# Performance work log

Hardware: AMD Instinct MI355X
Metric: run time of the kernel (lower is better)

The kernel has to match this reference:

```python
import jax, jax.numpy as jnp
import numpy as np

B, S, T = 256, 512, 20
VOCAB, E, H, SKIP = 100000, 25, 128, 64


def _lstm_scan(x, skip, mask, K, R, Sk, b):
    # x:[S,B,E], skip:[S,B,SKIP], mask:[S,B] bool. Keras RNN mask semantics:
    # masked steps carry previous h/c and emit previous h.
    Bn = x.shape[1]
    Hn = R.shape[0]
    def step(carry, inp):
        h, c = carry
        xt, st, mt = inp
        z = xt @ K + h @ R + st @ Sk + b            # [B,4H]
        zi, zf, zg, zo = jnp.split(z, 4, axis=-1)
        cn = jax.nn.sigmoid(zf) * c + jax.nn.sigmoid(zi) * jnp.tanh(zg)
        hn = jax.nn.sigmoid(zo) * jnp.tanh(cn)
        m = mt[:, None]
        h2 = jnp.where(m, hn, h)
        c2 = jnp.where(m, cn, c)
        return (h2, c2), h2
    init = (jnp.zeros((Bn, Hn), x.dtype), jnp.zeros((Bn, Hn), x.dtype))
    (hF, cF), hs = jax.lax.scan(step, init, (x, skip, mask))
    return hs, hF


def setup_inputs() -> dict:
    key = jax.random.key(0)
    ks = jax.random.split(key, 20)
    p = lambda k, shp: jax.random.normal(k, shp, dtype=jnp.float32) * 0.05
    inp = {
        "input_tags": jax.random.randint(ks[0], (B, S, T), 0, VOCAB, dtype=jnp.int32),
        "embedded_skips": jax.random.normal(ks[1], (B, S, SKIP), dtype=jnp.float32),
        "emb_table": p(ks[2], (VOCAB, E)),
        "kernel_f": p(ks[3], (E, 4 * H)),
        "rec_f": p(ks[4], (H, 4 * H)),
        "skip_f": p(ks[5], (SKIP, 4 * H)),
        "bias_f": jnp.zeros((4 * H,), jnp.float32),
        "kernel_b": p(ks[6], (E, 4 * H)),
        "rec_b": p(ks[7], (H, 4 * H)),
        "skip_b": p(ks[8], (SKIP, 4 * H)),
        "bias_b": jnp.zeros((4 * H,), jnp.float32),
        "Wk": p(ks[9], (2 * H, H)),
        "bk": jnp.zeros((H,), jnp.float32),
        "Wq": p(ks[10], (H, H)),
        "bq": jnp.zeros((H,), jnp.float32),
        "We": p(ks[11], (H, 1)),
        "be": jnp.zeros((1,), jnp.float32),
    }
    return inp


def reference(input_tags, embedded_skips, emb_table,
              kernel_f, rec_f, skip_f, bias_f,
              kernel_b, rec_b, skip_b, bias_b,
              Wk, bk, Wq, bq, We, be):
    mask3 = input_tags != 0                          # [B,S,T]
    emb = emb_table[input_tags]                      # [B,S,T,E]
    num_mask = mask3.astype(emb.dtype)
    summed = jnp.sum(emb * num_mask[..., None], axis=2)   # [B,S,E]
    denom = jnp.sum(num_mask, axis=2)                     # [B,S]
    denom = jnp.where(denom == 0, jnp.ones_like(denom), denom)
    gru_inp = summed / denom[..., None]                   # [B,S,E]
    step_mask = mask3[:, :, 0]                            # [B,S]

    # time-major for scan
    x_t = jnp.swapaxes(gru_inp, 0, 1)
    s_t = jnp.swapaxes(embedded_skips, 0, 1)
    m_t = jnp.swapaxes(step_mask, 0, 1)

    hs_f, h_fwd = _lstm_scan(x_t, s_t, m_t, kernel_f, rec_f, skip_f, bias_f)
    hs_b_rev, _ = _lstm_scan(x_t[::-1], s_t[::-1], m_t[::-1], kernel_b, rec_b, skip_b, bias_b)
    hs_b = hs_b_rev[::-1]
    out = jnp.swapaxes(jnp.concatenate([hs_f, hs_b], axis=-1), 0, 1)  # [B,S,2H]

    keys = out @ Wk + bk                                  # [B,S,H]
    queries = (h_fwd @ Wq + bq)[:, None, :]               # [B,1,H]
    energy = jnp.tanh(keys + queries) @ We + be           # [B,S,1]
    energy = energy + (1.0 - step_mask.astype(energy.dtype))[..., None] * -1e9
    weights = jax.nn.softmax(energy, axis=1)
    context = jnp.sum(weights * out, axis=1)              # [B,2H]
    return context
```

## Files before the change

### kernel.cpp

```cpp
#include <hip/hip_runtime.h>
#include <math.h>

#define Bb 256
#define Ss 512
#define Tt 20
#define Ee 25
#define Hh 128
#define SKIPn 64
#define H4n 512
#define BSn (Bb*Ss)
#define MG 4
#define HP 160
#define ZP 520
#define AP 264
#define LOG2E 1.4426950408889634f

typedef _Float16 f16x8 __attribute__((ext_vector_type(8)));
typedef _Float16 f16x4 __attribute__((ext_vector_type(4)));
typedef float f32x4 __attribute__((ext_vector_type(4)));

__device__ __forceinline__ float rcpf(float x) { return __builtin_amdgcn_rcpf(x); }
__device__ __forceinline__ float exp2f_(float x) { return __builtin_amdgcn_exp2f(x); }

__device__ __forceinline__ void lgkm_barrier() {
    __asm__ __volatile__("" ::: "memory");
    __builtin_amdgcn_s_waitcnt(0xC07F);
    __builtin_amdgcn_s_barrier();
    __asm__ __volatile__("" ::: "memory");
}

__global__ void pool_kernel(const int* __restrict__ tags,
                            const float* __restrict__ table,
                            _Float16* __restrict__ gru16, float* __restrict__ maskf,
                            float* __restrict__ maskt) {
    int group = blockIdx.x * 8 + (threadIdx.x >> 5);
    int lane = threadIdx.x & 31;
    if (group >= BSn) return;
    int b = group >> 9;
    int t = group & (Ss - 1);
    const int* tg = tags + (size_t)group * Tt;
    const int el = (lane < Ee) ? lane : (Ee - 1);

    int tagv[Tt];
#pragma unroll
    for (int tt = 0; tt < Tt; tt++) tagv[tt] = tg[tt];

    float vv[Tt];
#pragma unroll
    for (int tt = 0; tt < Tt; tt++)
        vv[tt] = table[(size_t)tagv[tt] * Ee + el];

    float acc = 0.0f;
    int cnt = 0;
#pragma unroll
    for (int tt = 0; tt < Tt; tt++) {
        const bool nz = (tagv[tt] != 0);
        cnt += nz ? 1 : 0;
        acc += nz ? vv[tt] : 0.0f;
    }
    float scale = rcpf((float)(cnt > 0 ? cnt : 1));
    float v = (lane < Ee) ? acc * scale : 0.0f;
    gru16[((size_t)t * Bb + b) * 32 + lane] = (_Float16)v;
    if (lane == 0) {
        float m = (tagv[0] != 0) ? 1.0f : 0.0f;
        maskf[group] = m;
        maskt[(size_t)t * Bb + b] = m;
    }
}

__global__ void __launch_bounds__(256)
cvt_kernel(const float* __restrict__ in, _Float16* __restrict__ out) {
    size_t i = ((size_t)blockIdx.x * 256 + threadIdx.x) * 8;
    f32x4 a = *(const f32x4*)(in + i);
    f32x4 b = *(const f32x4*)(in + i + 4);
    f16x8 o;
#pragma unroll
    for (int j = 0; j < 4; j++) { o[j] = (_Float16)a[j]; o[j + 4] = (_Float16)b[j]; }
    *(f16x8*)(out + i) = o;
}

__global__ void __launch_bounds__(512)
__attribute__((amdgpu_waves_per_eu(2, 2)))
scan_kernel(const _Float16* __restrict__ gru16, const _Float16* __restrict__ sk16,
            const float* __restrict__ maskt,
            const float* __restrict__ Kf, const float* __restrict__ Rf,
            const float* __restrict__ Skf, const float* __restrict__ bf,
            const float* __restrict__ Kb, const float* __restrict__ Rb,
            const float* __restrict__ Skb, const float* __restrict__ bb,
            _Float16* __restrict__ hs16, float* __restrict__ hfwd)
{
    __shared__ __align__(16) _Float16 h16[2 * MG * HP];
    __shared__ __align__(16) _Float16 zlds[64 * ZP];

    const int tid = threadIdx.x;
    const int lane = tid & 63;
    const int w = tid >> 6;
    const int l16 = lane & 15;
    const int q = lane >> 4;
    const int mb = l16 >> 2;
    const int bg = blockIdx.x & 63;
    const int dir = blockIdx.x >> 6;
    const int b0 = bg * MG;
    const int col = 16 * w + l16;

    const float* Kw = dir ? Kb : Kf;
    const float* Rw = dir ? Rb : Rf;
    const float* Sw = dir ? Skb : Skf;
    const float* bw = dir ? bb : bf;
    const float gs[4] = {LOG2E, LOG2E, 2.0f * LOG2E, LOG2E};

    f16x8 hfr[4][4];
#pragma unroll
    for (int kt = 0; kt < 4; kt++) {
#pragma unroll
        for (int g = 0; g < 4; g++) {
            const int n = g * Hh + col;
            f16x8 v;
#pragma unroll
            for (int j = 0; j < 8; j++)
                v[j] = (_Float16)(Rw[(32 * kt + 8 * q + j) * H4n + n] * gs[g]);
            hfr[kt][g] = v;
        }
    }
    f16x8 bx[4], bs0[4], bs1[4];
    f32x4 biasA[4];
#pragma unroll
    for (int g = 0; g < 4; g++) {
        const int n = g * Hh + col;
        f16x8 vx, v0, v1;
#pragma unroll
        for (int j = 0; j < 8; j++) {
            const int kk = 8 * q + j;
            vx[j] = (_Float16)(((kk < Ee) ? Kw[kk * H4n + n] : 0.0f) * gs[g]);
            v0[j] = (_Float16)(Sw[kk * H4n + n] * gs[g]);
            v1[j] = (_Float16)(Sw[(32 + kk) * H4n + n] * gs[g]);
        }
        bx[g] = vx; bs0[g] = v0; bs1[g] = v1;
        const float bv = bw[g * Hh + col] * gs[g];
        f32x4 ba = {bv, bv, bv, bv};
        biasA[g] = ba;
    }
    const f32x4 zacc4 = {0.0f, 0.0f, 0.0f, 0.0f};

    for (int idx = tid; idx < 2 * MG * HP; idx += 512) h16[idx] = (_Float16)0.0f;

    float c = 0.0f, h = 0.0f;

    const int tsub = l16 >> 2, bbn = l16 & 3;
    const int tg0 = dir ? (Ss - 1 - tsub) : tsub;
    const _Float16* px = gru16 + ((size_t)tg0 * Bb + b0 + bbn) * 32 + 8 * q;
    const _Float16* ps = sk16 + ((size_t)(b0 + bbn) * Ss + tg0) * SKIPn + 8 * q;
    const ptrdiff_t pxd = (dir ? -4 : 4) * (ptrdiff_t)(Bb * 32);
    const ptrdiff_t psd = (dir ? -4 : 4) * (ptrdiff_t)SKIPn;

    const float* mptr = maskt + (size_t)(dir ? (Ss - 1) : 0) * Bb + b0 + q;
    const ptrdiff_t mdelta = dir ? -(ptrdiff_t)Bb : (ptrdiff_t)Bb;
    float mA = mptr[0], mB = mptr[mdelta];
    const float* mpf = mptr + 2 * mdelta;

    _Float16* hsp = hs16 + ((size_t)(b0 + q) * Ss + (dir ? Ss - 1 : 0)) * (2 * Hh)
                    + dir * Hh + col;
    const ptrdiff_t odelta = dir ? -(2 * Hh) : (2 * Hh);

    f16x8 nax = *(const f16x8*)px;
    f16x8 na0 = *(const f16x8*)ps;
    f16x8 na1 = *(const f16x8*)(ps + 32);

    __syncthreads();

    auto body = [&](int i, float& mkv) {
        const _Float16* hb = h16 + (i & 1) * (MG * HP);
        const f16x8 ah0 = *(const f16x8*)(hb + mb * HP +  0 + 8 * q);
        const f16x8 ah1 = *(const f16x8*)(hb + mb * HP + 32 + 8 * q);
        const f16x8 ah2 = *(const f16x8*)(hb + mb * HP + 64 + 8 * q);
        const f16x8 ah3 = *(const f16x8*)(hb + mb * HP + 96 + 8 * q);
        const f16x4 z4 = *(const f16x4*)(zlds + ((i & 15) * 4 + q) * ZP + col * 4);

        f32x4 acc[4];
#pragma unroll
        for (int g = 0; g < 4; g++) {
            acc[g] = __builtin_amdgcn_mfma_f32_16x16x32_f16(ah0, hfr[0][g], zacc4, 0, 0, 0);
            acc[g] = __builtin_amdgcn_mfma_f32_16x16x32_f16(ah1, hfr[1][g], acc[g], 0, 0, 0);
            acc[g] = __builtin_amdgcn_mfma_f32_16x16x32_f16(ah2, hfr[2][g], acc[g], 0, 0, 0);
            acc[g] = __builtin_amdgcn_mfma_f32_16x16x32_f16(ah3, hfr[3][g], acc[g], 0, 0, 0);
        }

        const float mk = mkv;
        mkv = *mpf; mpf += mdelta;
        const float zi = acc[0][0] + (float)z4[0];
        const float zf = acc[1][0] + (float)z4[1];
        const float zg = acc[2][0] + (float)z4[2];
        const float zo = acc[3][0] + (float)z4[3];
        const float ei = exp2f_(fminf(-zi, 88.0f));
        const float ef = exp2f_(fminf(-zf, 88.0f));
        const float eg = exp2f_(fminf(-zg, 88.0f));
        const float eo = exp2f_(fminf(-zo, 88.0f));
        const float pi = 1.0f + ei, pg = 1.0f + eg, pf = 1.0f + ef;
        const float p  = pi * pg;
        const float t1 = (1.0f - eg) * pf;
        const float cn = fmaf(c, p, t1) * rcpf(pf * p);
        const float ec = exp2f_(fminf(cn * (-2.0f * LOG2E), 88.0f));
        const float hn = (1.0f - ec) * rcpf((1.0f + eo) * (1.0f + ec));
        const bool mm = (mk != 0.0f);
        c = mm ? cn : c;
        h = mm ? hn : h;

        _Float16* hw = h16 + ((i + 1) & 1) * (MG * HP);
        hw[q * HP + col] = (_Float16)h;
        *hsp = (_Float16)h;
        hsp += odelta;
        lgkm_barrier();
    };

    int i = 0;
#pragma unroll 1
    for (int k = 0; k < 32; ++k) {
#pragma unroll
        for (int tile = 0; tile < 4; ++tile) {
            const f16x8 ax = nax, a0 = na0, a1 = na1;
            px += pxd; ps += psd;
            if ((k < 31) | (tile < 3)) {
                nax = *(const f16x8*)px;
                na0 = *(const f16x8*)ps;
                na1 = *(const f16x8*)(ps + 32);
            }
            f32x4 zc[4];
#pragma unroll
            for (int g = 0; g < 4; g++) {
                zc[g] = __builtin_amdgcn_mfma_f32_16x16x32_f16(ax, bx[g],  biasA[g], 0, 0, 0);
                zc[g] = __builtin_amdgcn_mfma_f32_16x16x32_f16(a0, bs0[g], zc[g], 0, 0, 0);
                zc[g] = __builtin_amdgcn_mfma_f32_16x16x32_f16(a1, bs1[g], zc[g], 0, 0, 0);
            }
            _Float16* zw = zlds + ((tile * 4 + q) * 4) * ZP + col * 4;
#pragma unroll
            for (int r = 0; r < 4; r++) {
                f16x4 o;
                o[0] = (_Float16)zc[0][r]; o[1] = (_Float16)zc[1][r];
                o[2] = (_Float16)zc[2][r]; o[3] = (_Float16)zc[3][r];
                *(f16x4*)(zw + r * ZP) = o;
            }
        }
        lgkm_barrier();
#pragma unroll 1
        for (int j = 0; j < 16; j += 2) {
            body(i,     mA);
            body(i + 1, mB);
            i += 2;
        }
    }

    if (dir == 0) hfwd[(size_t)(b0 + q) * Hh + col] = h;
}

__global__ void __launch_bounds__(512)
attn_kernel(const _Float16* __restrict__ hs16, const float* __restrict__ hfwd,
            const float* __restrict__ Wq, const float* __restrict__ bq,
            const float* __restrict__ bk,
            const float* __restrict__ Wk, const float* __restrict__ We,
            const float* __restrict__ maskf, float* __restrict__ outp)
{
    __shared__ float hfl[Hh];
    __shared__ float qpart[4][Hh];
    __shared__ float qtot_s[Hh];
    __shared__ float epart[8][Ss];
    __shared__ float ws2[Ss];
    __shared__ float redm[8], reds[8];
    __shared__ float ctxp[16][2 * Hh + 1];
    __shared__ __align__(16) _Float16 atile[2][16 * AP];

    const int tid = threadIdx.x;
    const int lane = tid & 63;
    const int w = tid >> 6;
    const int l16 = lane & 15;
    const int q = lane >> 4;
    const int b = blockIdx.x;
    const int j = 16 * w + l16;

    f16x8 bk16[8];
#pragma unroll
    for (int kt = 0; kt < 8; kt++) {
        f16x8 v;
#pragma unroll
        for (int jj = 0; jj < 8; jj++)
            v[jj] = (_Float16)Wk[(32 * kt + 8 * q + jj) * Hh + j];
        bk16[kt] = v;
    }
    const float wej = We[j];

    if (tid < Hh) hfl[tid] = hfwd[(size_t)b * Hh + tid];
    __syncthreads();
    {
        const int jj = tid & 127, seg = tid >> 7;
        float p = 0.0f;
#pragma unroll
        for (int k = 0; k < 32; k++)
            p += hfl[32 * seg + k] * Wq[(32 * seg + k) * Hh + jj];
        qpart[seg][jj] = p;
    }
    __syncthreads();
    if (tid < Hh)
        qtot_s[tid] = qpart[0][tid] + qpart[1][tid] + qpart[2][tid] + qpart[3][tid]
                      + bq[tid] + bk[tid];
    __syncthreads();
    const float qj = qtot_s[j];

    const _Float16* hb = hs16 + (size_t)b * Ss * (2 * Hh);
    const int srow = tid >> 5;
    const int spart = tid & 31;
    *(f16x8*)(&atile[0][srow * AP + spart * 8]) =
        *(const f16x8*)(hb + (size_t)srow * (2 * Hh) + spart * 8);
    __syncthreads();
#pragma unroll 1
    for (int st = 0; st < 32; st++) {
        const int p = st & 1;
        f16x8 sreg;
        if (st < 31)
            sreg = *(const f16x8*)(hb + (size_t)((st + 1) * 16 + srow) * (2 * Hh) + spart * 8);
        const int s0 = st * 16;
        f32x4 acc = {0.f, 0.f, 0.f, 0.f};
#pragma unroll
        for (int kt = 0; kt < 8; kt++) {
            const f16x8 a = *(const f16x8*)(&atile[p][l16 * AP + kt * 32 + 8 * q]);
            acc = __builtin_amdgcn_mfma_f32_16x16x32_f16(a, bk16[kt], acc, 0, 0, 0);
        }
        float vals[4];
#pragma unroll
        for (int r = 0; r < 4; r++) {
            const float x = acc[r] + qj;
            const float e = exp2f_(fminf(x * (-2.0f * LOG2E), 80.0f));
            vals[r] = (1.0f - e) * rcpf(1.0f + e) * wej;
        }
#pragma unroll
        for (int m = 1; m < 16; m <<= 1) {
#pragma unroll
            for (int r = 0; r < 4; r++) vals[r] += __shfl_xor(vals[r], m);
        }
        if (l16 == 0) {
#pragma unroll
            for (int r = 0; r < 4; r++) epart[w][s0 + 4 * q + r] = vals[r];
        }
        if (st < 31)
            *(f16x8*)(&atile[p ^ 1][srow * AP + spart * 8]) = sreg;
        __syncthreads();
    }

    {
        float e = 0.0f;
#pragma unroll
        for (int ww = 0; ww < 8; ww++) e += epart[ww][tid];
        e += (1.0f - maskf[(size_t)b * Ss + tid]) * -1e9f;
        float mx = e;
#pragma unroll
        for (int off = 32; off > 0; off >>= 1) mx = fmaxf(mx, __shfl_xor(mx, off));
        if (lane == 0) redm[w] = mx;
        __syncthreads();
        mx = redm[0];
#pragma unroll
        for (int ww = 1; ww < 8; ww++) mx = fmaxf(mx, redm[ww]);
        const float p = exp2f_((e - mx) * LOG2E);
        float sm = p;
#pragma unroll
        for (int off = 32; off > 0; off >>= 1) sm += __shfl_xor(sm, off);
        if (lane == 0) reds[w] = sm;
        __syncthreads();
        sm = reds[0] + reds[1] + reds[2] + reds[3] + reds[4] + reds[5] + reds[6] + reds[7];
        ws2[(tid & 31) * 16 + (tid >> 5)] = p * rcpf(sm);
    }
    __syncthreads();

    {
        const int cg = tid & 31;
        const int seg = tid >> 5;
        float a[8];
#pragma unroll
        for (int jj = 0; jj < 8; jj++) a[jj] = 0.0f;
#pragma unroll 4
        for (int sg = 0; sg < 32; sg++) {
            const int s = seg * 32 + sg;
            const float wv = ws2[sg * 16 + seg];
            const f16x8 hv = *(const f16x8*)(hb + (size_t)s * (2 * Hh) + 8 * cg);
#pragma unroll
            for (int jj = 0; jj < 8; jj++) a[jj] = fmaf(wv, (float)hv[jj], a[jj]);
        }
#pragma unroll
        for (int jj = 0; jj < 8; jj++) ctxp[seg][8 * cg + jj] = a[jj];
    }
    __syncthreads();
    if (tid < 2 * Hh) {
        float s = 0.0f;
#pragma unroll
        for (int seg = 0; seg < 16; seg++) s += ctxp[seg][tid];
        outp[(size_t)b * (2 * Hh) + tid] = s;
    }
}

extern "C" void kernel_launch(void* const* d_in, const int* in_sizes, int n_in,
                              void* d_out, int out_size, void* d_ws, size_t ws_size,
                              hipStream_t stream) {
    const int*   tags  = (const int*)d_in[0];
    const float* skips = (const float*)d_in[1];
    const float* table = (const float*)d_in[2];
    const float* Kf    = (const float*)d_in[3];
    const float* Rf    = (const float*)d_in[4];
    const float* Skf   = (const float*)d_in[5];
    const float* bf    = (const float*)d_in[6];
    const float* Kb    = (const float*)d_in[7];
    const float* Rb    = (const float*)d_in[8];
    const float* Skb   = (const float*)d_in[9];
    const float* bb    = (const float*)d_in[10];
    const float* Wk    = (const float*)d_in[11];
    const float* bk    = (const float*)d_in[12];
    const float* Wq    = (const float*)d_in[13];
    const float* bq    = (const float*)d_in[14];
    const float* We    = (const float*)d_in[15];

    char* ws = (char*)d_ws;
    _Float16* gru16 = (_Float16*)ws; ws += (size_t)BSn * 32 * 2;
    _Float16* sk16  = (_Float16*)ws; ws += (size_t)BSn * SKIPn * 2;
    float* maskf = (float*)ws; ws += (size_t)BSn * 4;
    float* maskt_base = (float*)ws; ws += ((size_t)BSn + 4 * Bb) * 4;
    float* maskt = maskt_base + 2 * Bb;
    _Float16* hs16 = (_Float16*)ws; ws += (size_t)BSn * 2 * Hh * 2;
    float* hfwd  = (float*)ws; ws += (size_t)Bb * Hh * 4;

    pool_kernel<<<BSn / 8, 256, 0, stream>>>(tags, table, gru16, maskf, maskt);
    cvt_kernel<<<BSn * SKIPn / (256 * 8), 256, 0, stream>>>(skips, sk16);
    scan_kernel<<<128, 512, 0, stream>>>(gru16, sk16, maskt,
                                         Kf, Rf, Skf, bf,
                                         Kb, Rb, Skb, bb,
                                         hs16, hfwd);
    attn_kernel<<<Bb, 512, 0, stream>>>(hs16, hfwd, Wq, bq, bk, Wk, We, maskf,
                                        (float*)d_out);
}
```

Measured before the change: 539.7 us.

## Interleave input-projection MFMAs into recurrent steps with double-buffered z tiles

```diff
diff --git a/kernel.cpp b/kernel.cpp
--- a/kernel.cpp
+++ b/kernel.cpp
@@ -90,7 +90,7 @@
             _Float16* __restrict__ hs16, float* __restrict__ hfwd)
 {
     __shared__ __align__(16) _Float16 h16[2 * MG * HP];
-    __shared__ __align__(16) _Float16 zlds[64 * ZP];
+    __shared__ __align__(16) _Float16 zlds[2][16 * 4 * ZP];
 
     const int tid = threadIdx.x;
     const int lane = tid & 63;
@@ -150,102 +150,126 @@
     const int tg0 = dir ? (Ss - 1 - tsub) : tsub;
     const _Float16* px = gru16 + ((size_t)tg0 * Bb + b0 + bbn) * 32 + 8 * q;
     const _Float16* ps = sk16 + ((size_t)(b0 + bbn) * Ss + tg0) * SKIPn + 8 * q;
-    const ptrdiff_t pxd = (dir ? -4 : 4) * (ptrdiff_t)(Bb * 32);
-    const ptrdiff_t psd = (dir ? -4 : 4) * (ptrdiff_t)SKIPn;
-
-    const float* mptr = maskt + (size_t)(dir ? (Ss - 1) : 0) * Bb + b0 + q;
+    ptrdiff_t pxd = (dir ? -4 : 4) * (ptrdiff_t)(Bb * 32);
+    ptrdiff_t psd = (dir ? -4 : 4) * (ptrdiff_t)SKIPn;
+
+    const float* mpf = maskt + (size_t)(dir ? (Ss - 1) : 0) * Bb + b0 + q;
     const ptrdiff_t mdelta = dir ? -(ptrdiff_t)Bb : (ptrdiff_t)Bb;
-    float mA = mptr[0], mB = mptr[mdelta];
-    const float* mpf = mptr + 2 * mdelta;
+    float mreg[2];
+    mreg[0] = mpf[0]; mreg[1] = mpf[mdelta];
+    mpf += 2 * mdelta;
 
     _Float16* hsp = hs16 + ((size_t)(b0 + q) * Ss + (dir ? Ss - 1 : 0)) * (2 * Hh)
                     + dir * Hh + col;
     const ptrdiff_t odelta = dir ? -(2 * Hh) : (2 * Hh);
 
-    f16x8 nax = *(const f16x8*)px;
-    f16x8 na0 = *(const f16x8*)ps;
-    f16x8 na1 = *(const f16x8*)(ps + 32);
-
-    __syncthreads();
-
-    auto body = [&](int i, float& mkv) {
-        const _Float16* hb = h16 + (i & 1) * (MG * HP);
-        const f16x8 ah0 = *(const f16x8*)(hb + mb * HP +  0 + 8 * q);
-        const f16x8 ah1 = *(const f16x8*)(hb + mb * HP + 32 + 8 * q);
-        const f16x8 ah2 = *(const f16x8*)(hb + mb * HP + 64 + 8 * q);
-        const f16x8 ah3 = *(const f16x8*)(hb + mb * HP + 96 + 8 * q);
-        const f16x4 z4 = *(const f16x4*)(zlds + ((i & 15) * 4 + q) * ZP + col * 4);
-
-        f32x4 acc[4];
+    f16x8 gx, g0, g1;
+    auto ldA = [&]() {
+        gx = *(const f16x8*)px;
+        g0 = *(const f16x8*)ps;
+        g1 = *(const f16x8*)(ps + 32);
+        px += pxd; ps += psd;
+    };
+
+    f32x4 zc[4];
+
+    ldA();
+#pragma unroll
+    for (int T = 0; T < 4; T++) {
+        const f16x8 ax = gx, a0 = g0, a1 = g1;
+        ldA();
 #pragma unroll
         for (int g = 0; g < 4; g++) {
-            acc[g] = __builtin_amdgcn_mfma_f32_16x16x32_f16(ah0, hfr[0][g], zacc4, 0, 0, 0);
-            acc[g] = __builtin_amdgcn_mfma_f32_16x16x32_f16(ah1, hfr[1][g], acc[g], 0, 0, 0);
-            acc[g] = __builtin_amdgcn_mfma_f32_16x16x32_f16(ah2, hfr[2][g], acc[g], 0, 0, 0);
-            acc[g] = __builtin_amdgcn_mfma_f32_16x16x32_f16(ah3, hfr[3][g], acc[g], 0, 0, 0);
-        }
-
-        const float mk = mkv;
-        mkv = *mpf; mpf += mdelta;
-        const float zi = acc[0][0] + (float)z4[0];
-        const float zf = acc[1][0] + (float)z4[1];
-        const float zg = acc[2][0] + (float)z4[2];
-        const float zo = acc[3][0] + (float)z4[3];
-        const float ei = exp2f_(fminf(-zi, 88.0f));
-        const float ef = exp2f_(fminf(-zf, 88.0f));
-        const float eg = exp2f_(fminf(-zg, 88.0f));
-        const float eo = exp2f_(fminf(-zo, 88.0f));
-        const float pi = 1.0f + ei, pg = 1.0f + eg, pf = 1.0f + ef;
-        const float p  = pi * pg;
-        const float t1 = (1.0f - eg) * pf;
-        const float cn = fmaf(c, p, t1) * rcpf(pf * p);
-        const float ec = exp2f_(fminf(cn * (-2.0f * LOG2E), 88.0f));
-        const float hn = (1.0f - ec) * rcpf((1.0f + eo) * (1.0f + ec));
-        const bool mm = (mk != 0.0f);
-        c = mm ? cn : c;
-        h = mm ? hn : h;
-
-        _Float16* hw = h16 + ((i + 1) & 1) * (MG * HP);
-        hw[q * HP + col] = (_Float16)h;
-        *hsp = (_Float16)h;
-        hsp += odelta;
-        lgkm_barrier();
-    };
-
-    int i = 0;
+            zc[g] = __builtin_amdgcn_mfma_f32_16x16x32_f16(ax, bx[g],  biasA[g], 0, 0, 0);
+            zc[g] = __builtin_amdgcn_mfma_f32_16x16x32_f16(a0, bs0[g], zc[g], 0, 0, 0);
+            zc[g] = __builtin_amdgcn_mfma_f32_16x16x32_f16(a1, bs1[g], zc[g], 0, 0, 0);
+        }
+        _Float16* zw = &zlds[0][0] + ((4 * T + q) * 4) * ZP + col * 4;
+#pragma unroll
+        for (int r = 0; r < 4; r++) {
+            f16x4 o;
+            o[0] = (_Float16)zc[0][r]; o[1] = (_Float16)zc[1][r];
+            o[2] = (_Float16)zc[2][r]; o[3] = (_Float16)zc[3][r];
+            *(f16x4*)(zw + r * ZP) = o;
+        }
+    }
+    __syncthreads();
+
 #pragma unroll 1
     for (int k = 0; k < 32; ++k) {
-#pragma unroll
-        for (int tile = 0; tile < 4; ++tile) {
-            const f16x8 ax = nax, a0 = na0, a1 = na1;
-            px += pxd; ps += psd;
-            if ((k < 31) | (tile < 3)) {
-                nax = *(const f16x8*)px;
-                na0 = *(const f16x8*)ps;
-                na1 = *(const f16x8*)(ps + 32);
+        const _Float16* zr = &zlds[k & 1][0];
+        _Float16* zwb = &zlds[(k + 1) & 1][0];
+
+#pragma unroll
+        for (int j = 0; j < 16; ++j) {
+            const int T = j >> 2, ph = j & 3;
+
+            const _Float16* hb = h16 + (j & 1) * (MG * HP);
+            const f16x8 ah0 = *(const f16x8*)(hb + mb * HP +  0 + 8 * q);
+            const f16x8 ah1 = *(const f16x8*)(hb + mb * HP + 32 + 8 * q);
+            const f16x8 ah2 = *(const f16x8*)(hb + mb * HP + 64 + 8 * q);
+            const f16x8 ah3 = *(const f16x8*)(hb + mb * HP + 96 + 8 * q);
+            const f16x4 z4 = *(const f16x4*)(zr + (j * 4 + q) * ZP + col * 4);
+
+            f32x4 accA[4], accB[4];
+#pragma unroll
+            for (int g = 0; g < 4; g++) {
+                accA[g] = __builtin_amdgcn_mfma_f32_16x16x32_f16(ah0, hfr[0][g], zacc4, 0, 0, 0);
+                accB[g] = __builtin_amdgcn_mfma_f32_16x16x32_f16(ah1, hfr[1][g], zacc4, 0, 0, 0);
+                accA[g] = __builtin_amdgcn_mfma_f32_16x16x32_f16(ah2, hfr[2][g], accA[g], 0, 0, 0);
+                accB[g] = __builtin_amdgcn_mfma_f32_16x16x32_f16(ah3, hfr[3][g], accB[g], 0, 0, 0);
             }
-            f32x4 zc[4];
-#pragma unroll
-            for (int g = 0; g < 4; g++) {
-                zc[g] = __builtin_amdgcn_mfma_f32_16x16x32_f16(ax, bx[g],  biasA[g], 0, 0, 0);
-                zc[g] = __builtin_amdgcn_mfma_f32_16x16x32_f16(a0, bs0[g], zc[g], 0, 0, 0);
-                zc[g] = __builtin_amdgcn_mfma_f32_16x16x32_f16(a1, bs1[g], zc[g], 0, 0, 0);
+
+            if (ph == 0) {
+#pragma unroll
+                for (int g = 0; g < 4; g++)
+                    zc[g] = __builtin_amdgcn_mfma_f32_16x16x32_f16(gx, bx[g], biasA[g], 0, 0, 0);
+            } else if (ph == 1) {
+#pragma unroll
+                for (int g = 0; g < 4; g++)
+                    zc[g] = __builtin_amdgcn_mfma_f32_16x16x32_f16(g0, bs0[g], zc[g], 0, 0, 0);
+            } else if (ph == 2) {
+#pragma unroll
+                for (int g = 0; g < 4; g++)
+                    zc[g] = __builtin_amdgcn_mfma_f32_16x16x32_f16(g1, bs1[g], zc[g], 0, 0, 0);
+                if (j == 10 && k == 30) { pxd = 0; psd = 0; }
+                ldA();
+            } else {
+                _Float16* zw = zwb + ((4 * T + q) * 4) * ZP + col * 4;
+#pragma unroll
+                for (int r = 0; r < 4; r++) {
+                    f16x4 o;
+                    o[0] = (_Float16)zc[0][r]; o[1] = (_Float16)zc[1][r];
+                    o[2] = (_Float16)zc[2][r]; o[3] = (_Float16)zc[3][r];
+                    *(f16x4*)(zw + r * ZP) = o;
+                }
             }
-            _Float16* zw = zlds + ((tile * 4 + q) * 4) * ZP + col * 4;
-#pragma unroll
-            for (int r = 0; r < 4; r++) {
-                f16x4 o;
-                o[0] = (_Float16)zc[0][r]; o[1] = (_Float16)zc[1][r];
-                o[2] = (_Float16)zc[2][r]; o[3] = (_Float16)zc[3][r];
-                *(f16x4*)(zw + r * ZP) = o;
-            }
-        }
-        lgkm_barrier();
-#pragma unroll 1
-        for (int j = 0; j < 16; j += 2) {
-            body(i,     mA);
-            body(i + 1, mB);
-            i += 2;
+
+            const float mk = mreg[j & 1];
+            mreg[j & 1] = *mpf; mpf += mdelta;
+            const float zi = accA[0][0] + accB[0][0] + (float)z4[0];
+            const float zf = accA[1][0] + accB[1][0] + (float)z4[1];
+            const float zg = accA[2][0] + accB[2][0] + (float)z4[2];
+            const float zo = accA[3][0] + accB[3][0] + (float)z4[3];
+            const float ei = exp2f_(-zi);
+            const float ef = exp2f_(-zf);
+            const float eg = exp2f_(-zg);
+            const float eo = exp2f_(-zo);
+            const float pi = 1.0f + ei, pg = 1.0f + eg, pf = 1.0f + ef;
+            const float p  = pi * pg;
+            const float t1 = (1.0f - eg) * pf;
+            const float cn = fmaf(c, p, t1) * rcpf(pf * p);
+            const float ec = exp2f_(cn * (-2.0f * LOG2E));
+            const float hn = (1.0f - ec) * rcpf((1.0f + eo) * (1.0f + ec));
+            const bool mm = (mk != 0.0f);
+            c = mm ? cn : c;
+            h = mm ? hn : h;
+
+            _Float16* hw = h16 + ((j + 1) & 1) * (MG * HP);
+            hw[q * HP + col] = (_Float16)h;
+            *hsp = (_Float16)h;
+            hsp += odelta;
+            lgkm_barrier();
         }
     }
 
```

Measured after the change: 467.3 us. -13.4%, faster.
